# Kernel tuning notes

Measured on AMD Instinct MI355X. Metric: run time of the kernel, lower is better.

## Reference

```python
import jax, jax.numpy as jnp
import numpy as np

N_NODES = 50000
N_EDGES = 800000
NFEAT, NHID, NCLASS = 512, 64, 40


def setup_inputs() -> dict:
    key = jax.random.key(0)
    ks = jax.random.split(key, 10)
    x = jax.random.normal(ks[0], (N_NODES, NFEAT), dtype=jnp.float32)
    edge_weight = jax.random.uniform(ks[1], (N_EDGES,), dtype=jnp.float32)
    W1 = jax.random.normal(ks[2], (NFEAT, NHID), dtype=jnp.float32) / np.sqrt(NFEAT)
    b1 = jnp.zeros((NHID,), dtype=jnp.float32)
    W2 = jax.random.normal(ks[3], (NHID, NHID), dtype=jnp.float32) / np.sqrt(NHID)
    b2 = jnp.zeros((NHID,), dtype=jnp.float32)
    W3 = jax.random.normal(ks[4], (NHID, NCLASS), dtype=jnp.float32) / np.sqrt(NHID)
    b3 = jnp.zeros((NCLASS,), dtype=jnp.float32)
    row = jax.random.randint(ks[5], (N_EDGES,), 0, N_NODES, dtype=jnp.int32)
    col = jax.random.randint(ks[6], (N_EDGES,), 0, N_NODES, dtype=jnp.int32)
    return {"x": x, "edge_weight": edge_weight, "W1": W1, "b1": b1,
            "W2": W2, "b2": b2, "W3": W3, "b3": b3, "row": row, "col": col}


def _gcn_layer(h, W, b, row, col, ew):
    # support = h @ W + b ; out = spmm(adj, support)
    support = h @ W + b                      # [N, dout]
    msg = support[col] * ew[:, None]         # gather + scale, [E, dout]
    return jax.ops.segment_sum(msg, row, num_segments=N_NODES)


def reference(x, edge_weight, W1, b1, W2, b2, W3, b3, row, col):
    h = jax.nn.relu(_gcn_layer(x, W1, b1, row, col, edge_weight))
    # dropout: eval mode -> identity
    h = _gcn_layer(h, W2, b2, row, col, edge_weight)
    h = _gcn_layer(h, W3, b3, row, col, edge_weight)
    return jax.nn.log_softmax(h, axis=1)
```

## Files before the change

### kernel.cpp

```cpp
#include <hip/hip_runtime.h>
#include <hip/hip_bf16.h>

#define NNODES 50000
#define NEDGES 800000
#define NFEAT  512
#define NHID   64
#define NCLASS 40

#define CAP 48
#define CNTSTRIDE 16
#define EPT 4
#define FILL_BLOCKS ((NEDGES / EPT + 255) / 256)
#define GEMM1_BLOCKS ((NNODES + 31) / 32)

typedef __attribute__((ext_vector_type(8))) short short8;
typedef __attribute__((ext_vector_type(4))) float floatx4;

static __device__ __forceinline__ unsigned short f2bf(float f) {
    union { float f; unsigned u; } v; v.f = f;
    const unsigned r = v.u + 0x7fffu + ((v.u >> 16) & 1u);
    return (unsigned short)(r >> 16);
}
static __device__ __forceinline__ float bf2f(unsigned u) {
    union { unsigned u; float f; } v; v.u = u << 16;
    return v.f;
}

template<int NCB, int NVALID>
static __device__ __forceinline__ void convW_body(
    const float* __restrict__ W, unsigned short* __restrict__ wb, int idx) {
    const int lane = idx & 63;
    const int cb   = (idx >> 6) % NCB;
    const int kb   = idx / (64 * NCB);
    const int q = lane >> 4, m = lane & 15;
    const int c = cb * 16 + m;
    short8 v;
    #pragma unroll
    for (int j = 0; j < 8; ++j)
        v[j] = (c < NVALID)
             ? (short)f2bf(W[(size_t)(kb * 32 + q * 8 + j) * NVALID + c])
             : (short)0;
    *(short8*)(wb + (size_t)idx * 8) = v;
}

__global__ __launch_bounds__(256) void conv_kernel(
    const float* __restrict__ W1, unsigned short* __restrict__ wb1,
    const float* __restrict__ W2, unsigned short* __restrict__ wb2,
    const float* __restrict__ W3, unsigned short* __restrict__ wb3,
    int4* __restrict__ cnt4) {
    const int blk = blockIdx.x;
    const int tid = threadIdx.x;
    if (blk < 16) {
        convW_body<4, 64>(W1, wb1, blk * 256 + tid);
    } else if (blk < 18) {
        convW_body<4, 64>(W2, wb2, (blk - 16) * 256 + tid);
    } else if (blk < 20) {
        const int idx = (blk - 18) * 256 + tid;
        if (idx < 2 * 3 * 64) convW_body<3, 40>(W3, wb3, idx);
    } else {
        const int i = (blk - 20) * 256 + tid;
        if (i < NNODES * CNTSTRIDE / 4) cnt4[i] = make_int4(0, 0, 0, 0);
    }
}

__global__ __launch_bounds__(256) void fill_kernel(
    const int* __restrict__ row, const int* __restrict__ col,
    const float* __restrict__ ew, int* __restrict__ cnt,
    unsigned* __restrict__ bucket) {
    const int e = (blockIdx.x * 256 + threadIdx.x) * EPT;
    if (e >= NEDGES) return;
    const int4   r4 = *(const int4*)(row + e);
    const int4   c4 = *(const int4*)(col + e);
    const float4 w4 = *(const float4*)(ew + e);
    const int p0 = atomicAdd(&cnt[r4.x * CNTSTRIDE], 1);
    const int p1 = atomicAdd(&cnt[r4.y * CNTSTRIDE], 1);
    const int p2 = atomicAdd(&cnt[r4.z * CNTSTRIDE], 1);
    const int p3 = atomicAdd(&cnt[r4.w * CNTSTRIDE], 1);
    if (p0 < CAP) bucket[(size_t)r4.x * CAP + p0] = (unsigned)c4.x | ((unsigned)f2bf(w4.x) << 16);
    if (p1 < CAP) bucket[(size_t)r4.y * CAP + p1] = (unsigned)c4.y | ((unsigned)f2bf(w4.y) << 16);
    if (p2 < CAP) bucket[(size_t)r4.z * CAP + p2] = (unsigned)c4.z | ((unsigned)f2bf(w4.z) << 16);
    if (p3 < CAP) bucket[(size_t)r4.w * CAP + p3] = (unsigned)c4.w | ((unsigned)f2bf(w4.w) << 16);
}

__global__ __launch_bounds__(256) void gemm1_kernel(
    const float* __restrict__ x, const unsigned short* __restrict__ wb,
    const float* __restrict__ b, unsigned short* __restrict__ outb) {
    const int g = blockIdx.x;
    const int tid = threadIdx.x;
    __shared__ float red[2][16][64];

    const int lane = tid & 63;
    const int wid  = tid >> 6;
    const int p  = wid >> 1;
    const int kh = wid & 1;
    const int q = lane >> 4, m = lane & 15;

    const int rowbase = g * 32 + p * 16;
    int rload = rowbase + m;
    if (rload >= NNODES) rload = NNODES - 1;
    const float* xp = x + (size_t)rload * NFEAT + kh * 256 + q * 8;

    floatx4 acc[4];
    #pragma unroll
    for (int cb = 0; cb < 4; ++cb) acc[cb] = (floatx4)0.f;

    #pragma unroll
    for (int kc = 0; kc < 2; ++kc) {
        float4 a0[4], a1[4];
        #pragma unroll
        for (int u = 0; u < 4; ++u) {
            a0[u] = *(const float4*)(xp + (kc * 4 + u) * 32);
            a1[u] = *(const float4*)(xp + (kc * 4 + u) * 32 + 4);
        }
        #pragma unroll
        for (int u = 0; u < 4; ++u) {
            short8 afrag;
            afrag[0] = (short)f2bf(a0[u].x); afrag[1] = (short)f2bf(a0[u].y);
            afrag[2] = (short)f2bf(a0[u].z); afrag[3] = (short)f2bf(a0[u].w);
            afrag[4] = (short)f2bf(a1[u].x); afrag[5] = (short)f2bf(a1[u].y);
            afrag[6] = (short)f2bf(a1[u].z); afrag[7] = (short)f2bf(a1[u].w);

            const int kbg = kh * 8 + kc * 4 + u;
            const unsigned short* wp = wb + ((size_t)(kbg * 4) * 64 + lane) * 8;
            #pragma unroll
            for (int cb = 0; cb < 4; ++cb) {
                const short8 bfrag = *(const short8*)(wp + (size_t)cb * 64 * 8);
                acc[cb] = __builtin_amdgcn_mfma_f32_16x16x32_bf16(
                    afrag, bfrag, acc[cb], 0, 0, 0);
            }
        }
    }

    if (kh == 1) {
        #pragma unroll
        for (int cb = 0; cb < 4; ++cb)
            #pragma unroll
            for (int i = 0; i < 4; ++i)
                red[p][q * 4 + i][cb * 16 + m] = acc[cb][i];
    }
    __syncthreads();
    if (kh == 1) return;

    const int orow = rowbase + q * 4;
    #pragma unroll
    for (int cb = 0; cb < 4; ++cb) {
        const int c = cb * 16 + m;
        const float bias = b[c];
        #pragma unroll
        for (int i = 0; i < 4; ++i) {
            const int rr2 = orow + i;
            if (rr2 < NNODES)
                outb[(size_t)rr2 * NHID + c] =
                    f2bf(acc[cb][i] + red[p][q * 4 + i][c] + bias);
        }
    }
}

template<bool RELU, int NCB, int NOUT>
__global__ __launch_bounds__(256) void spmm_gemm_kernel(
    const unsigned short* __restrict__ supb, const unsigned* __restrict__ bucket,
    const int* __restrict__ cnt, const unsigned short* __restrict__ wb,
    const float* __restrict__ bias, unsigned short* __restrict__ outb) {
    __shared__ unsigned short ht[4 * 72];

    const int tid  = threadIdx.x;
    const int wid  = tid >> 6;
    const int lane = tid & 63;
    const int half = lane >> 5;
    const int fp   = lane & 31;
    const int n    = blockIdx.x * 4 + wid;

    float a0 = 0.f, a1 = 0.f;
    if (n < NNODES) {
        int deg = cnt[n * CNTSTRIDE];
        if (deg > CAP) deg = CAP;
        const unsigned* ep = bucket + (size_t)n * CAP;
        for (int i = half; i < deg; i += 16) {
            unsigned eb[8], vb[8];
            #pragma unroll
            for (int j = 0; j < 8; ++j) {
                const int idx = i + 2 * j;
                eb[j] = (idx < deg) ? ep[idx] : 0u;
            }
            #pragma unroll
            for (int j = 0; j < 8; ++j)
                vb[j] = *(const unsigned*)(supb + (size_t)(eb[j] & 0xffffu) * NHID + fp * 2);
            #pragma unroll
            for (int j = 0; j < 8; ++j) {
                const float w = bf2f(eb[j] >> 16);
                a0 += w * bf2f(vb[j] & 0xffffu);
                a1 += w * bf2f(vb[j] >> 16);
            }
        }
    }
    a0 += __shfl_xor(a0, 32);
    a1 += __shfl_xor(a1, 32);
    if (RELU) { a0 = fmaxf(a0, 0.f); a1 = fmaxf(a1, 0.f); }
    if (half == 0)
        *(unsigned*)&ht[wid * 72 + fp * 2] =
            (unsigned)f2bf(a0) | ((unsigned)f2bf(a1) << 16);
    __syncthreads();

    if (wid != 0) return;
    const int q = lane >> 4, m = lane & 15;
    const unsigned short* hp = &ht[(m & 3) * 72 + q * 8];

    floatx4 acc[NCB];
    #pragma unroll
    for (int cb = 0; cb < NCB; ++cb) acc[cb] = (floatx4)0.f;

    #pragma unroll
    for (int kb = 0; kb < 2; ++kb) {
        const short8 afrag = *(const short8*)(hp + kb * 32);
        const unsigned short* wp = wb + ((size_t)(kb * NCB) * 64 + lane) * 8;
        #pragma unroll
        for (int cb = 0; cb < NCB; ++cb) {
            const short8 bfrag = *(const short8*)(wp + (size_t)cb * 64 * 8);
            acc[cb] = __builtin_amdgcn_mfma_f32_16x16x32_bf16(
                afrag, bfrag, acc[cb], 0, 0, 0);
        }
    }

    if (q != 0) return;
    #pragma unroll
    for (int cb = 0; cb < NCB; ++cb) {
        const int c = cb * 16 + m;
        if (c >= NOUT) continue;
        const float bv = bias[c];
        #pragma unroll
        for (int i = 0; i < 4; ++i) {
            const int r = blockIdx.x * 4 + i;
            if (r < NNODES)
                outb[(size_t)r * NOUT + c] = f2bf(acc[cb][i] + bv);
        }
    }
}

__global__ __launch_bounds__(256) void spmm_bf40_lsm_kernel(
    const unsigned short* __restrict__ supb, const unsigned* __restrict__ bucket,
    const int* __restrict__ cnt, float* __restrict__ out) {
    const int f = threadIdx.x & 63;
    const int n = blockIdx.x * 4 + (threadIdx.x >> 6);
    if (n >= NNODES) return;
    int deg = cnt[n * CNTSTRIDE];
    if (deg > CAP) deg = CAP;
    const unsigned* ep = bucket + (size_t)n * CAP;
    float acc = 0.f;
    if (f < NCLASS) {
        for (int i = 0; i < deg; i += 8) {
            unsigned eb[8]; float vb[8];
            #pragma unroll
            for (int j = 0; j < 8; ++j) {
                const int idx = i + j;
                eb[j] = (idx < deg) ? ep[idx] : 0u;
            }
            #pragma unroll
            for (int j = 0; j < 8; ++j)
                vb[j] = bf2f(supb[(size_t)(eb[j] & 0xffffu) * NCLASS + f]);
            #pragma unroll
            for (int j = 0; j < 8; ++j)
                acc += vb[j] * bf2f(eb[j] >> 16);
        }
    }
    float m = (f < NCLASS) ? acc : -1e30f;
    #pragma unroll
    for (int o = 32; o > 0; o >>= 1) m = fmaxf(m, __shfl_xor(m, o));
    float ex = (f < NCLASS) ? __expf(acc - m) : 0.f;
    #pragma unroll
    for (int o = 32; o > 0; o >>= 1) ex += __shfl_xor(ex, o);
    const float ls = __logf(ex) + m;
    if (f < NCLASS) out[(size_t)n * NCLASS + f] = acc - ls;
}

extern "C" void kernel_launch(void* const* d_in, const int* in_sizes, int n_in,
                              void* d_out, int out_size, void* d_ws, size_t ws_size,
                              hipStream_t stream) {
    const float* x  = (const float*)d_in[0];
    const float* ew = (const float*)d_in[1];
    const float* W1 = (const float*)d_in[2];
    const float* b1 = (const float*)d_in[3];
    const float* W2 = (const float*)d_in[4];
    const float* b2 = (const float*)d_in[5];
    const float* W3 = (const float*)d_in[6];
    const float* b3 = (const float*)d_in[7];
    const int* row  = (const int*)d_in[8];
    const int* col  = (const int*)d_in[9];
    float* out = (float*)d_out;

    const size_t n64 = (size_t)NNODES * NHID;
    const size_t n40 = (size_t)NNODES * NCLASS;
    unsigned* bucket = (unsigned*)d_ws;
    int* cnt = (int*)(bucket + (size_t)NNODES * CAP);
    unsigned short* S1 = (unsigned short*)(cnt + (size_t)NNODES * CNTSTRIDE);
    unsigned short* S2 = S1 + n64;
    unsigned short* S3 = S2 + n64;
    unsigned short* wb1 = S3 + n40;
    unsigned short* wb2 = wb1 + 16 * 4 * 64 * 8;
    unsigned short* wb3 = wb2 + 2 * 4 * 64 * 8;

    const int nodeBlocks = (NNODES + 3) / 4;

    conv_kernel<<<820, 256, 0, stream>>>(W1, wb1, W2, wb2, W3, wb3, (int4*)cnt);

    fill_kernel<<<FILL_BLOCKS, 256, 0, stream>>>(row, col, ew, cnt, bucket);

    gemm1_kernel<<<GEMM1_BLOCKS, 256, 0, stream>>>(x, wb1, b1, S1);

    spmm_gemm_kernel<true, 4, 64><<<nodeBlocks, 256, 0, stream>>>(
        S1, bucket, cnt, wb2, b2, S2);

    spmm_gemm_kernel<false, 3, 40><<<nodeBlocks, 256, 0, stream>>>(
        S2, bucket, cnt, wb3, b3, S3);

    spmm_bf40_lsm_kernel<<<nodeBlocks, 256, 0, stream>>>(S3, bucket, cnt, out);
}
```

Measured before the change: 320.6 us.

## Merge bucket fill with gemm1 and batch four nodes per wave in spmm

New measurement: 288.1 us. -10.1%, faster.

```diff
diff --git a/kernel.cpp b/kernel.cpp
--- a/kernel.cpp
+++ b/kernel.cpp
@@ -10,8 +10,9 @@
 #define CAP 48
 #define CNTSTRIDE 16
 #define EPT 4
-#define FILL_BLOCKS ((NEDGES / EPT + 255) / 256)
+#define FILL_CHUNKS ((NEDGES / EPT + 255) / 256)
 #define GEMM1_BLOCKS ((NNODES + 31) / 32)
+#define SPMM_BLOCKS ((NNODES + 15) / 16)
 
 typedef __attribute__((ext_vector_type(8))) short short8;
 typedef __attribute__((ext_vector_type(4))) float floatx4;
@@ -63,30 +64,36 @@
     }
 }
 
-__global__ __launch_bounds__(256) void fill_kernel(
+__global__ __launch_bounds__(256) void bucket_gemm1_kernel(
     const int* __restrict__ row, const int* __restrict__ col,
     const float* __restrict__ ew, int* __restrict__ cnt,
-    unsigned* __restrict__ bucket) {
-    const int e = (blockIdx.x * 256 + threadIdx.x) * EPT;
-    if (e >= NEDGES) return;
-    const int4   r4 = *(const int4*)(row + e);
-    const int4   c4 = *(const int4*)(col + e);
-    const float4 w4 = *(const float4*)(ew + e);
-    const int p0 = atomicAdd(&cnt[r4.x * CNTSTRIDE], 1);
-    const int p1 = atomicAdd(&cnt[r4.y * CNTSTRIDE], 1);
-    const int p2 = atomicAdd(&cnt[r4.z * CNTSTRIDE], 1);
-    const int p3 = atomicAdd(&cnt[r4.w * CNTSTRIDE], 1);
-    if (p0 < CAP) bucket[(size_t)r4.x * CAP + p0] = (unsigned)c4.x | ((unsigned)f2bf(w4.x) << 16);
-    if (p1 < CAP) bucket[(size_t)r4.y * CAP + p1] = (unsigned)c4.y | ((unsigned)f2bf(w4.y) << 16);
-    if (p2 < CAP) bucket[(size_t)r4.z * CAP + p2] = (unsigned)c4.z | ((unsigned)f2bf(w4.z) << 16);
-    if (p3 < CAP) bucket[(size_t)r4.w * CAP + p3] = (unsigned)c4.w | ((unsigned)f2bf(w4.w) << 16);
-}
-
-__global__ __launch_bounds__(256) void gemm1_kernel(
+    unsigned* __restrict__ bucket,
     const float* __restrict__ x, const unsigned short* __restrict__ wb,
     const float* __restrict__ b, unsigned short* __restrict__ outb) {
-    const int g = blockIdx.x;
-    const int tid = threadIdx.x;
+    const int blk  = blockIdx.x;
+    const int tid  = threadIdx.x;
+    const int base = blk / 3;
+    const int r    = blk % 3;
+
+    if (r == 2) {
+        const int e = (base * 256 + tid) * EPT;
+        if (e >= NEDGES) return;
+        const int4   r4 = *(const int4*)(row + e);
+        const int4   c4 = *(const int4*)(col + e);
+        const float4 w4 = *(const float4*)(ew + e);
+        const int p0 = atomicAdd(&cnt[r4.x * CNTSTRIDE], 1);
+        const int p1 = atomicAdd(&cnt[r4.y * CNTSTRIDE], 1);
+        const int p2 = atomicAdd(&cnt[r4.z * CNTSTRIDE], 1);
+        const int p3 = atomicAdd(&cnt[r4.w * CNTSTRIDE], 1);
+        if (p0 < CAP) bucket[(size_t)r4.x * CAP + p0] = (unsigned)c4.x | ((unsigned)f2bf(w4.x) << 16);
+        if (p1 < CAP) bucket[(size_t)r4.y * CAP + p1] = (unsigned)c4.y | ((unsigned)f2bf(w4.y) << 16);
+        if (p2 < CAP) bucket[(size_t)r4.z * CAP + p2] = (unsigned)c4.z | ((unsigned)f2bf(w4.z) << 16);
+        if (p3 < CAP) bucket[(size_t)r4.w * CAP + p3] = (unsigned)c4.w | ((unsigned)f2bf(w4.w) << 16);
+        return;
+    }
+
+    const int g = base * 2 + r;
+    if (g >= GEMM1_BLOCKS) return;
     __shared__ float red[2][16][64];
 
     const int lane = tid & 63;
@@ -161,49 +168,68 @@
     const unsigned short* __restrict__ supb, const unsigned* __restrict__ bucket,
     const int* __restrict__ cnt, const unsigned short* __restrict__ wb,
     const float* __restrict__ bias, unsigned short* __restrict__ outb) {
-    __shared__ unsigned short ht[4 * 72];
+    __shared__ unsigned short ht[16 * 72];
 
     const int tid  = threadIdx.x;
     const int wid  = tid >> 6;
     const int lane = tid & 63;
     const int half = lane >> 5;
     const int fp   = lane & 31;
-    const int n    = blockIdx.x * 4 + wid;
-
-    float a0 = 0.f, a1 = 0.f;
-    if (n < NNODES) {
-        int deg = cnt[n * CNTSTRIDE];
-        if (deg > CAP) deg = CAP;
-        const unsigned* ep = bucket + (size_t)n * CAP;
-        for (int i = half; i < deg; i += 16) {
-            unsigned eb[8], vb[8];
-            #pragma unroll
-            for (int j = 0; j < 8; ++j) {
+    const int nb   = blockIdx.x * 16 + wid * 4;
+
+    float a0[4] = {0.f, 0.f, 0.f, 0.f}, a1[4] = {0.f, 0.f, 0.f, 0.f};
+    int deg[4]; const unsigned* ep[4];
+    int maxd = 0;
+    #pragma unroll
+    for (int jn = 0; jn < 4; ++jn) {
+        const int n = nb + jn;
+        int d = (n < NNODES) ? cnt[n * CNTSTRIDE] : 0;
+        if (d > CAP) d = CAP;
+        deg[jn] = d;
+        maxd = max(maxd, d);
+        ep[jn] = bucket + (size_t)(n < NNODES ? n : 0) * CAP;
+    }
+
+    for (int i = half; i < maxd; i += 8) {
+        unsigned eb[4][4], vb[4][4];
+        #pragma unroll
+        for (int jn = 0; jn < 4; ++jn)
+            #pragma unroll
+            for (int j = 0; j < 4; ++j) {
                 const int idx = i + 2 * j;
-                eb[j] = (idx < deg) ? ep[idx] : 0u;
+                eb[jn][j] = (idx < deg[jn]) ? ep[jn][idx] : 0u;
             }
-            #pragma unroll
-            for (int j = 0; j < 8; ++j)
-                vb[j] = *(const unsigned*)(supb + (size_t)(eb[j] & 0xffffu) * NHID + fp * 2);
-            #pragma unroll
-            for (int j = 0; j < 8; ++j) {
-                const float w = bf2f(eb[j] >> 16);
-                a0 += w * bf2f(vb[j] & 0xffffu);
-                a1 += w * bf2f(vb[j] >> 16);
+        #pragma unroll
+        for (int jn = 0; jn < 4; ++jn)
+            #pragma unroll
+            for (int j = 0; j < 4; ++j)
+                vb[jn][j] = *(const unsigned*)(supb + (size_t)(eb[jn][j] & 0xffffu) * NHID + fp * 2);
+        #pragma unroll
+        for (int jn = 0; jn < 4; ++jn)
+            #pragma unroll
+            for (int j = 0; j < 4; ++j) {
+                const float w = bf2f(eb[jn][j] >> 16);
+                a0[jn] += w * bf2f(vb[jn][j] & 0xffffu);
+                a1[jn] += w * bf2f(vb[jn][j] >> 16);
             }
-        }
-    }
-    a0 += __shfl_xor(a0, 32);
-    a1 += __shfl_xor(a1, 32);
-    if (RELU) { a0 = fmaxf(a0, 0.f); a1 = fmaxf(a1, 0.f); }
-    if (half == 0)
-        *(unsigned*)&ht[wid * 72 + fp * 2] =
-            (unsigned)f2bf(a0) | ((unsigned)f2bf(a1) << 16);
+    }
+    #pragma unroll
+    for (int jn = 0; jn < 4; ++jn) {
+        a0[jn] += __shfl_xor(a0[jn], 32);
+        a1[jn] += __shfl_xor(a1[jn], 32);
+        if (RELU) { a0[jn] = fmaxf(a0[jn], 0.f); a1[jn] = fmaxf(a1[jn], 0.f); }
+    }
+    if (half == 0) {
+        #pragma unroll
+        for (int jn = 0; jn < 4; ++jn)
+            *(unsigned*)&ht[(wid * 4 + jn) * 72 + fp * 2] =
+                (unsigned)f2bf(a0[jn]) | ((unsigned)f2bf(a1[jn]) << 16);
+    }
     __syncthreads();
 
     if (wid != 0) return;
     const int q = lane >> 4, m = lane & 15;
-    const unsigned short* hp = &ht[(m & 3) * 72 + q * 8];
+    const unsigned short* hp = &ht[m * 72 + q * 8];
 
     floatx4 acc[NCB];
     #pragma unroll
@@ -221,7 +247,7 @@
         }
     }
 
-    if (q != 0) return;
+    const int rbase = blockIdx.x * 16 + q * 4;
     #pragma unroll
     for (int cb = 0; cb < NCB; ++cb) {
         const int c = cb * 16 + m;
@@ -229,9 +255,9 @@
         const float bv = bias[c];
         #pragma unroll
         for (int i = 0; i < 4; ++i) {
-            const int r = blockIdx.x * 4 + i;
-            if (r < NNODES)
-                outb[(size_t)r * NOUT + c] = f2bf(acc[cb][i] + bv);
+            const int rr = rbase + i;
+            if (rr < NNODES)
+                outb[(size_t)rr * NOUT + c] = f2bf(acc[cb][i] + bv);
         }
     }
 }
@@ -247,18 +273,18 @@
     const unsigned* ep = bucket + (size_t)n * CAP;
     float acc = 0.f;
     if (f < NCLASS) {
-        for (int i = 0; i < deg; i += 8) {
-            unsigned eb[8]; float vb[8];
-            #pragma unroll
-            for (int j = 0; j < 8; ++j) {
+        for (int i = 0; i < deg; i += 16) {
+            unsigned eb[16]; float vb[16];
+            #pragma unroll
+            for (int j = 0; j < 16; ++j) {
                 const int idx = i + j;
                 eb[j] = (idx < deg) ? ep[idx] : 0u;
             }
             #pragma unroll
-            for (int j = 0; j < 8; ++j)
+            for (int j = 0; j < 16; ++j)
                 vb[j] = bf2f(supb[(size_t)(eb[j] & 0xffffu) * NCLASS + f]);
             #pragma unroll
-            for (int j = 0; j < 8; ++j)
+            for (int j = 0; j < 16; ++j)
                 acc += vb[j] * bf2f(eb[j] >> 16);
         }
     }
@@ -298,19 +324,16 @@
     unsigned short* wb2 = wb1 + 16 * 4 * 64 * 8;
     unsigned short* wb3 = wb2 + 2 * 4 * 64 * 8;
 
-    const int nodeBlocks = (NNODES + 3) / 4;
-
     conv_kernel<<<820, 256, 0, stream>>>(W1, wb1, W2, wb2, W3, wb3, (int4*)cnt);
 
-    fill_kernel<<<FILL_BLOCKS, 256, 0, stream>>>(row, col, ew, cnt, bucket);
-
-    gemm1_kernel<<<GEMM1_BLOCKS, 256, 0, stream>>>(x, wb1, b1, S1);
-
-    spmm_gemm_kernel<true, 4, 64><<<nodeBlocks, 256, 0, stream>>>(
+    bucket_gemm1_kernel<<<3 * FILL_CHUNKS, 256, 0, stream>>>(
+        row, col, ew, cnt, bucket, x, wb1, b1, S1);
+
+    spmm_gemm_kernel<true, 4, 64><<<SPMM_BLOCKS, 256, 0, stream>>>(
         S1, bucket, cnt, wb2, b2, S2);
 
-    spmm_gemm_kernel<false, 3, 40><<<nodeBlocks, 256, 0, stream>>>(
+    spmm_gemm_kernel<false, 3, 40><<<SPMM_BLOCKS, 256, 0, stream>>>(
         S2, bucket, cnt, wb3, b3, S3);
 
-    spmm_bf40_lsm_kernel<<<nodeBlocks, 256, 0, stream>>>(S3, bucket, cnt, out);
-}
+    spmm_bf40_lsm_kernel<<<(NNODES + 3) / 4, 256, 0, stream>>>(S3, bucket, cnt, out);
+}
```
